# Optimization experiments

Hardware: AMD Instinct MI355X
Metric: run time of the kernel (lower is better)

The kernel has to match this reference:

```python
import jax, jax.numpy as jnp
import numpy as np

N_NODES = 100000
N_EDGES = 1600000
N_GRAPHS = 256
IN_F = 64   # global_features (GNN input dim)
OUT_F = 64  # node_features (GNN output dim)


def setup_inputs() -> dict:
    key = jax.random.key(0)
    ks = jax.random.split(key, 8)
    x = jax.random.normal(ks[0], (N_NODES, IN_F), dtype=jnp.float32)
    edge_index = jax.random.randint(ks[1], (2, N_EDGES), 0, N_NODES, dtype=jnp.int64)
    batch = jnp.sort(jax.random.randint(ks[2], (N_NODES,), 0, N_GRAPHS, dtype=jnp.int64))
    # GNNLayer linear: in=global_features, out=node_features
    W_gnn = jax.random.normal(ks[3], (IN_F, OUT_F), dtype=jnp.float32) / np.sqrt(IN_F)
    b_gnn = jnp.zeros((OUT_F,), dtype=jnp.float32)
    # global_attention: Linear(node_features, 1)
    W_att = jax.random.normal(ks[4], (OUT_F, 1), dtype=jnp.float32) / np.sqrt(OUT_F)
    b_att = jnp.zeros((1,), dtype=jnp.float32)
    return {"x": x, "edge_index": edge_index, "batch": batch,
            "W_gnn": W_gnn, "b_gnn": b_gnn, "W_att": W_att, "b_att": b_att}


def reference(x, edge_index, batch, W_gnn, b_gnn, W_att, b_att):
    src, dst = edge_index[0], edge_index[1]
    # --- GNN message passing layer: aggregate neighbor features, transform ---
    agg = jax.ops.segment_sum(x[src], dst, num_segments=N_NODES)  # [N, IN_F]
    h = jax.nn.relu((x + agg) @ W_gnn + b_gnn)                    # [N, OUT_F]
    # --- attention scores + scatter softmax over batch segments ---
    scores = (h @ W_att + b_att)[:, 0]                            # [N]
    seg_max = jax.ops.segment_max(scores, batch, num_segments=N_GRAPHS)
    e = jnp.exp(scores - seg_max[batch])
    denom = jax.ops.segment_sum(e, batch, num_segments=N_GRAPHS)
    w = e / denom[batch]                                          # [N]
    # --- weighted scatter-add pooling ---
    out = jax.ops.segment_sum(w[:, None] * h, batch, num_segments=N_GRAPHS)
    return out  # [N_GRAPHS, OUT_F]
```

## Files before the change

### kernel.cpp

```cpp
#include <hip/hip_runtime.h>

#define N_NODES  100000
#define N_EDGES  1600000
#define N_GRAPHS 256
#define F        64

#define BSHIFT   8
#define BNODES   256
#define NBUCKET  391
#define CHUNK    8192
#define NCHUNK   196

__global__ __launch_bounds__(1024) void hist_kernel(
        const int* __restrict__ dst, int* __restrict__ cnt) {
    __shared__ int hist[NBUCKET];
    int tid = threadIdx.x;
    for (int b = tid; b < NBUCKET; b += 1024) hist[b] = 0;
    __syncthreads();
    int base = blockIdx.x * CHUNK;
    int end  = min(base + CHUNK, N_EDGES);
    for (int e = base + tid; e < end; e += 1024)
        atomicAdd(&hist[dst[e] >> BSHIFT], 1);
    __syncthreads();
    for (int b = tid; b < NBUCKET; b += 1024)
        cnt[blockIdx.x * NBUCKET + b] = hist[b];
}

__global__ __launch_bounds__(512) void chunk_scan_kernel(
        const int* __restrict__ cnt, int* __restrict__ start, int* __restrict__ bbase) {
    __shared__ int t[512];
    int b = threadIdx.x;
    int tot = 0;
    if (b < NBUCKET)
        for (int c = 0; c < NCHUNK; ++c) tot += cnt[c * NBUCKET + b];
    t[b] = (b < NBUCKET) ? tot : 0;
    __syncthreads();
    #pragma unroll
    for (int o = 1; o < 512; o <<= 1) {
        int u = (b >= o) ? t[b - o] : 0;
        __syncthreads();
        t[b] += u;
        __syncthreads();
    }
    if (b < NBUCKET) {
        int base = t[b] - tot;
        bbase[b] = base;
        if (b == NBUCKET - 1) bbase[NBUCKET] = t[b];
        int run = base;
        for (int c = 0; c < NCHUNK; ++c) {
            start[c * NBUCKET + b] = run;
            run += cnt[c * NBUCKET + b];
        }
    }
}

__global__ __launch_bounds__(1024) void scatter_kernel(
        const int* __restrict__ src, const int* __restrict__ dst,
        const int* __restrict__ start, unsigned int* __restrict__ pairs) {
    __shared__ int cur[NBUCKET];
    int tid = threadIdx.x;
    for (int b = tid; b < NBUCKET; b += 1024)
        cur[b] = start[blockIdx.x * NBUCKET + b];
    __syncthreads();
    int base = blockIdx.x * CHUNK;
    int end  = min(base + CHUNK, N_EDGES);
    for (int e = base + tid; e < end; e += 1024) {
        int d = dst[e];
        int slot = atomicAdd(&cur[d >> BSHIFT], 1);
        pairs[slot] = ((unsigned)(d & (BNODES - 1)) << 17) | (unsigned)src[e];
    }
}

__global__ __launch_bounds__(1024) void bucket_sort_kernel(
        const unsigned int* __restrict__ pairs,
        const int* __restrict__ bbase,
        int* __restrict__ eidx, int* __restrict__ noff) {
    __shared__ int cnt[BNODES];
    __shared__ int pref[BNODES];
    __shared__ int cur[BNODES];
    int tid = threadIdx.x;
    int b = blockIdx.x;
    int lo = bbase[b], hi = bbase[b + 1];

    if (tid < BNODES) cnt[tid] = 0;
    __syncthreads();
    for (int e = lo + tid; e < hi; e += 1024)
        atomicAdd(&cnt[pairs[e] >> 17], 1);
    __syncthreads();
    if (tid < BNODES) pref[tid] = cnt[tid];
    __syncthreads();
    #pragma unroll
    for (int o = 1; o < BNODES; o <<= 1) {
        int u = (tid < BNODES && tid >= o) ? pref[tid - o] : 0;
        __syncthreads();
        if (tid < BNODES) pref[tid] += u;
        __syncthreads();
    }
    if (tid < BNODES) {
        int excl = lo + pref[tid] - cnt[tid];
        cur[tid] = excl;
        int node = b * BNODES + tid;
        if (node < N_NODES) noff[node] = excl;
        if (node == N_NODES - 1) noff[N_NODES] = hi;
    }
    __syncthreads();
    for (int e = lo + tid; e < hi; e += 1024) {
        unsigned int p = pairs[e];
        int slot = atomicAdd(&cur[p >> 17], 1);
        eidx[slot] = (int)(p & 0x1FFFFu);
    }
}

#define NODES_PER_WAVE 25
#define GT_NWAVES  (N_NODES / NODES_PER_WAVE)
#define GT_BLOCKS  (GT_NWAVES / 4)

__global__ __launch_bounds__(256, 4) void gather_pool_kernel(
        const float* __restrict__ x,
        const int*   __restrict__ noff,
        const int*   __restrict__ eidx,
        const int*   __restrict__ batch,
        const float* __restrict__ Wg,
        const float* __restrict__ bg,
        const float* __restrict__ Wa,
        const float* __restrict__ ba,
        float*       __restrict__ out_acc,
        float*       __restrict__ denom) {
    int tid  = threadIdx.x;
    int lane = tid & 63;
    int grp  = lane >> 4;
    int c    = lane & 15;
    int waveId = blockIdx.x * 4 + (tid >> 6);

    float wcol[F];
    #pragma unroll
    for (int k = 0; k < F; ++k) wcol[k] = Wg[k * F + lane];
    float bgl = bg[lane];
    float wal = Wa[lane];
    float ba0 = ba[0];

    const float4* x4 = (const float4*)x;

    int n0   = waveId * NODES_PER_WAVE;
    int nEnd = n0 + NODES_PER_WAVE;

    int   cur_g = batch[n0];
    float accw  = 0.f;
    float denw  = 0.f;

    for (int n = n0; n < nEnd; ++n) {
        int start = noff[n];
        int end   = noff[n + 1];

        float4 a = make_float4(0.f, 0.f, 0.f, 0.f);
        for (int base = start; base < end; base += 64) {
            int jmax = end - base; if (jmax > 64) jmax = 64;
            int sl = (base + lane < end) ? eidx[base + lane] : 0;
            for (int j = 0; j < jmax; j += 4) {
                int el = j + grp;
                int s  = __shfl(sl, el, 64);
                if (el < jmax) {
                    float4 v = x4[s * 16 + c];
                    a.x += v.x; a.y += v.y; a.z += v.z; a.w += v.w;
                }
            }
        }
        #pragma unroll
        for (int o = 16; o <= 32; o <<= 1) {
            a.x += __shfl_xor(a.x, o, 64);
            a.y += __shfl_xor(a.y, o, 64);
            a.z += __shfl_xor(a.z, o, 64);
            a.w += __shfl_xor(a.w, o, 64);
        }
        { float4 v = x4[n * 16 + c]; a.x += v.x; a.y += v.y; a.z += v.z; a.w += v.w; }

        float re[4] = {a.x, a.y, a.z, a.w};
        float acc0 = 0.f, acc1 = 0.f, acc2 = 0.f, acc3 = 0.f;
        #pragma unroll
        for (int k = 0; k < F; k += 4) {
            float r0 = __int_as_float(__builtin_amdgcn_readlane(__float_as_int(re[0]), k >> 2));
            float r1 = __int_as_float(__builtin_amdgcn_readlane(__float_as_int(re[1]), k >> 2));
            float r2 = __int_as_float(__builtin_amdgcn_readlane(__float_as_int(re[2]), k >> 2));
            float r3 = __int_as_float(__builtin_amdgcn_readlane(__float_as_int(re[3]), k >> 2));
            acc0 += r0 * wcol[k + 0];
            acc1 += r1 * wcol[k + 1];
            acc2 += r2 * wcol[k + 2];
            acc3 += r3 * wcol[k + 3];
        }
        float hv = (acc0 + acc1) + (acc2 + acc3) + bgl;
        hv = hv > 0.f ? hv : 0.f;

        float p = hv * wal;
        #pragma unroll
        for (int o = 32; o > 0; o >>= 1)
            p += __shfl_down(p, o, 64);
        float s = __int_as_float(__builtin_amdgcn_readlane(__float_as_int(p), 0)) + ba0;
        float e = __expf(s);

        int g = batch[n];
        if (g != cur_g) {
            atomicAdd(&out_acc[cur_g * F + lane], accw);
            if (lane == 0) atomicAdd(&denom[cur_g], denw);
            accw = 0.f; denw = 0.f; cur_g = g;
        }
        accw += e * hv;
        denw += e;
    }
    atomicAdd(&out_acc[cur_g * F + lane], accw);
    if (lane == 0) atomicAdd(&denom[cur_g], denw);
}

__global__ __launch_bounds__(256) void finalize_kernel(
        float* __restrict__ out, const float* __restrict__ denom) {
    int i = blockIdx.x * 256 + threadIdx.x;
    if (i >= N_GRAPHS * F) return;
    float d = denom[i >> 6];
    out[i] = (d > 0.f) ? out[i] / d : 0.f;
}

extern "C" void kernel_launch(void* const* d_in, const int* in_sizes, int n_in,
                              void* d_out, int out_size, void* d_ws, size_t ws_size,
                              hipStream_t stream) {
    const float* x     = (const float*)d_in[0];
    const int*   ei    = (const int*)d_in[1];
    const int*   batch = (const int*)d_in[2];
    const float* Wg    = (const float*)d_in[3];
    const float* bg    = (const float*)d_in[4];
    const float* Wa    = (const float*)d_in[5];
    const float* ba    = (const float*)d_in[6];
    float* out = (float*)d_out;

    const int* src = ei;
    const int* dst = ei + N_EDGES;

    char* ws = (char*)d_ws;
    int*          cnt    = (int*)(ws);
    int*          start  = (int*)(ws +   306688);
    int*          bbase  = (int*)(ws +   613376);
    unsigned int* pairs  = (unsigned int*)(ws +  615168);
    int*          eidx   = (int*)(ws +  7015168);
    int*          noff   = (int*)(ws + 13415168);
    float*        denom  = (float*)(ws + 13815424);

    hipMemsetAsync(out,   0, (size_t)N_GRAPHS * F * sizeof(float), stream);
    hipMemsetAsync(denom, 0, N_GRAPHS * sizeof(float), stream);

    hist_kernel        <<<NCHUNK, 1024, 0, stream>>>(dst, cnt);
    chunk_scan_kernel  <<<1, 512, 0, stream>>>(cnt, start, bbase);
    scatter_kernel     <<<NCHUNK, 1024, 0, stream>>>(src, dst, start, pairs);
    bucket_sort_kernel <<<NBUCKET, 1024, 0, stream>>>(pairs, bbase, eidx, noff);
    gather_pool_kernel <<<GT_BLOCKS, 256, 0, stream>>>(
        x, noff, eidx, batch, Wg, bg, Wa, ba, out, denom);
    finalize_kernel    <<<(N_GRAPHS * F + 255) / 256, 256, 0, stream>>>(out, denom);
}
```

Measured before the change: 218.9 us.

## Gather neighbor features from a bf16 copy of x to halve gather bytes

Adds a cast kernel that writes x as bf16 into the workspace, and changes the gather kernel to read 16-byte packets of 8 bf16 values. Each 8-lane group now covers a full 64-feature row, so a wave processes 8 edges per step instead of 4. The readlane matmul is reworked for 8 accumulators, and the occupancy hint in launch bounds is dropped. The aim is to halve the random-gather traffic over about 1.6M edges, at the cost of an extra cast pass over x and a loss of precision that could push results past the tolerance.

```diff
diff --git a/kernel.cpp b/kernel.cpp
--- a/kernel.cpp
+++ b/kernel.cpp
@@ -10,6 +10,20 @@
 #define NBUCKET  391
 #define CHUNK    8192
 #define NCHUNK   196
+
+__device__ __forceinline__ unsigned short f2bf(float f) {
+    unsigned int u = __float_as_uint(f);
+    u += 0x7FFFu + ((u >> 16) & 1u);
+    return (unsigned short)(u >> 16);
+}
+__global__ __launch_bounds__(256) void cast_kernel(
+        const float* __restrict__ x, unsigned short* __restrict__ xh) {
+    int i = blockIdx.x * 256 + threadIdx.x;
+    float4 v = ((const float4*)x)[i];
+    ushort4 o;
+    o.x = f2bf(v.x); o.y = f2bf(v.y); o.z = f2bf(v.z); o.w = f2bf(v.w);
+    ((ushort4*)xh)[i] = o;
+}
 
 __global__ __launch_bounds__(1024) void hist_kernel(
         const int* __restrict__ dst, int* __restrict__ cnt) {
@@ -115,8 +129,15 @@
 #define GT_NWAVES  (N_NODES / NODES_PER_WAVE)
 #define GT_BLOCKS  (GT_NWAVES / 4)
 
-__global__ __launch_bounds__(256, 4) void gather_pool_kernel(
-        const float* __restrict__ x,
+__device__ __forceinline__ float bfl(unsigned int u) {
+    return __uint_as_float(u << 16);
+}
+__device__ __forceinline__ float bfh(unsigned int u) {
+    return __uint_as_float(u & 0xFFFF0000u);
+}
+
+__global__ __launch_bounds__(256) void gather_pool_kernel(
+        const unsigned short* __restrict__ xh,
         const int*   __restrict__ noff,
         const int*   __restrict__ eidx,
         const int*   __restrict__ batch,
@@ -128,9 +149,13 @@
         float*       __restrict__ denom) {
     int tid  = threadIdx.x;
     int lane = tid & 63;
-    int grp  = lane >> 4;
-    int c    = lane & 15;
+    int grp  = lane >> 3;
+    int c    = lane & 7;
     int waveId = blockIdx.x * 4 + (tid >> 6);
+
+    int n0 = waveId * NODES_PER_WAVE;
+    if (n0 >= N_NODES) return;
+    int nEnd = n0 + NODES_PER_WAVE;
 
     float wcol[F];
     #pragma unroll
@@ -139,10 +164,7 @@
     float wal = Wa[lane];
     float ba0 = ba[0];
 
-    const float4* x4 = (const float4*)x;
-
-    int n0   = waveId * NODES_PER_WAVE;
-    int nEnd = n0 + NODES_PER_WAVE;
+    const uint4* xh4 = (const uint4*)xh;
 
     int   cur_g = batch[n0];
     float accw  = 0.f;
@@ -152,42 +174,52 @@
         int start = noff[n];
         int end   = noff[n + 1];
 
-        float4 a = make_float4(0.f, 0.f, 0.f, 0.f);
+        float a0=0.f,a1=0.f,a2=0.f,a3=0.f,a4=0.f,a5=0.f,a6=0.f,a7=0.f;
         for (int base = start; base < end; base += 64) {
             int jmax = end - base; if (jmax > 64) jmax = 64;
             int sl = (base + lane < end) ? eidx[base + lane] : 0;
-            for (int j = 0; j < jmax; j += 4) {
+            for (int j = 0; j < jmax; j += 8) {
                 int el = j + grp;
                 int s  = __shfl(sl, el, 64);
                 if (el < jmax) {
-                    float4 v = x4[s * 16 + c];
-                    a.x += v.x; a.y += v.y; a.z += v.z; a.w += v.w;
+                    uint4 v = xh4[s * 8 + c];
+                    a0 += bfl(v.x); a1 += bfh(v.x);
+                    a2 += bfl(v.y); a3 += bfh(v.y);
+                    a4 += bfl(v.z); a5 += bfh(v.z);
+                    a6 += bfl(v.w); a7 += bfh(v.w);
                 }
             }
         }
         #pragma unroll
-        for (int o = 16; o <= 32; o <<= 1) {
-            a.x += __shfl_xor(a.x, o, 64);
-            a.y += __shfl_xor(a.y, o, 64);
-            a.z += __shfl_xor(a.z, o, 64);
-            a.w += __shfl_xor(a.w, o, 64);
-        }
-        { float4 v = x4[n * 16 + c]; a.x += v.x; a.y += v.y; a.z += v.z; a.w += v.w; }
-
-        float re[4] = {a.x, a.y, a.z, a.w};
-        float acc0 = 0.f, acc1 = 0.f, acc2 = 0.f, acc3 = 0.f;
+        for (int o = 8; o <= 32; o <<= 1) {
+            a0 += __shfl_xor(a0, o, 64); a1 += __shfl_xor(a1, o, 64);
+            a2 += __shfl_xor(a2, o, 64); a3 += __shfl_xor(a3, o, 64);
+            a4 += __shfl_xor(a4, o, 64); a5 += __shfl_xor(a5, o, 64);
+            a6 += __shfl_xor(a6, o, 64); a7 += __shfl_xor(a7, o, 64);
+        }
+        {
+            uint4 v = xh4[n * 8 + c];
+            a0 += bfl(v.x); a1 += bfh(v.x);
+            a2 += bfl(v.y); a3 += bfh(v.y);
+            a4 += bfl(v.z); a5 += bfh(v.z);
+            a6 += bfl(v.w); a7 += bfh(v.w);
+        }
+
+        float re[8] = {a0,a1,a2,a3,a4,a5,a6,a7};
+        float q0=0.f,q1=0.f,q2=0.f,q3=0.f,q4=0.f,q5=0.f,q6=0.f,q7=0.f;
         #pragma unroll
-        for (int k = 0; k < F; k += 4) {
-            float r0 = __int_as_float(__builtin_amdgcn_readlane(__float_as_int(re[0]), k >> 2));
-            float r1 = __int_as_float(__builtin_amdgcn_readlane(__float_as_int(re[1]), k >> 2));
-            float r2 = __int_as_float(__builtin_amdgcn_readlane(__float_as_int(re[2]), k >> 2));
-            float r3 = __int_as_float(__builtin_amdgcn_readlane(__float_as_int(re[3]), k >> 2));
-            acc0 += r0 * wcol[k + 0];
-            acc1 += r1 * wcol[k + 1];
-            acc2 += r2 * wcol[k + 2];
-            acc3 += r3 * wcol[k + 3];
-        }
-        float hv = (acc0 + acc1) + (acc2 + acc3) + bgl;
+        for (int k = 0; k < F; k += 8) {
+            int ln = k >> 3;
+            q0 += __int_as_float(__builtin_amdgcn_readlane(__float_as_int(re[0]), ln)) * wcol[k + 0];
+            q1 += __int_as_float(__builtin_amdgcn_readlane(__float_as_int(re[1]), ln)) * wcol[k + 1];
+            q2 += __int_as_float(__builtin_amdgcn_readlane(__float_as_int(re[2]), ln)) * wcol[k + 2];
+            q3 += __int_as_float(__builtin_amdgcn_readlane(__float_as_int(re[3]), ln)) * wcol[k + 3];
+            q4 += __int_as_float(__builtin_amdgcn_readlane(__float_as_int(re[4]), ln)) * wcol[k + 4];
+            q5 += __int_as_float(__builtin_amdgcn_readlane(__float_as_int(re[5]), ln)) * wcol[k + 5];
+            q6 += __int_as_float(__builtin_amdgcn_readlane(__float_as_int(re[6]), ln)) * wcol[k + 6];
+            q7 += __int_as_float(__builtin_amdgcn_readlane(__float_as_int(re[7]), ln)) * wcol[k + 7];
+        }
+        float hv = ((q0 + q1) + (q2 + q3)) + ((q4 + q5) + (q6 + q7)) + bgl;
         hv = hv > 0.f ? hv : 0.f;
 
         float p = hv * wal;
@@ -234,22 +266,24 @@
     const int* dst = ei + N_EDGES;
 
     char* ws = (char*)d_ws;
-    int*          cnt    = (int*)(ws);
-    int*          start  = (int*)(ws +   306688);
-    int*          bbase  = (int*)(ws +   613376);
-    unsigned int* pairs  = (unsigned int*)(ws +  615168);
-    int*          eidx   = (int*)(ws +  7015168);
-    int*          noff   = (int*)(ws + 13415168);
-    float*        denom  = (float*)(ws + 13815424);
+    int*            cnt    = (int*)(ws);
+    int*            start  = (int*)(ws +   306688);
+    int*            bbase  = (int*)(ws +   613376);
+    unsigned int*   pairs  = (unsigned int*)(ws +  615168);
+    int*            eidx   = (int*)(ws +  7015168);
+    int*            noff   = (int*)(ws + 13415168);
+    float*          denom  = (float*)(ws + 13815424);
+    unsigned short* xh     = (unsigned short*)(ws + 13816448);
 
     hipMemsetAsync(out,   0, (size_t)N_GRAPHS * F * sizeof(float), stream);
     hipMemsetAsync(denom, 0, N_GRAPHS * sizeof(float), stream);
 
+    cast_kernel        <<<(N_NODES * F / 4) / 256, 256, 0, stream>>>(x, xh);
     hist_kernel        <<<NCHUNK, 1024, 0, stream>>>(dst, cnt);
     chunk_scan_kernel  <<<1, 512, 0, stream>>>(cnt, start, bbase);
     scatter_kernel     <<<NCHUNK, 1024, 0, stream>>>(src, dst, start, pairs);
     bucket_sort_kernel <<<NBUCKET, 1024, 0, stream>>>(pairs, bbase, eidx, noff);
     gather_pool_kernel <<<GT_BLOCKS, 256, 0, stream>>>(
-        x, noff, eidx, batch, Wg, bg, Wa, ba, out, denom);
+        xh, noff, eidx, batch, Wg, bg, Wa, ba, out, denom);
     finalize_kernel    <<<(N_GRAPHS * F + 255) / 256, 256, 0, stream>>>(out, denom);
 }
```

Result: no change. 218.0 us (-0.4%).
